# Optimization experiments

Hardware: AMD Instinct MI355X
Metric: run time of the kernel (lower is better)

The kernel has to match this reference:

```python
import jax, jax.numpy as jnp
import numpy as np

B, T, D = 4, 1024, 768
HW = 32            # H = W = sqrt(T)
DS = D // 16       # d_state = 48
CHUNK = 8          # items_each_chunk (must divide W)


def _ln(x, w, b, eps=1e-5):
    mu = x.mean(-1, keepdims=True)
    var = ((x - mu) ** 2).mean(-1, keepdims=True)
    return (x - mu) / jnp.sqrt(var + eps) * w + b


def _conv1x1(x, w):  # x: (B,C,H,W), w: (O,C)
    return jnp.einsum('bchw,oc->bohw', x, w)


def _dwconv(x, w, b, pad):  # depthwise conv, w: (C,1,k,k)
    y = jax.lax.conv_general_dilated(
        x, w, (1, 1), [(pad, pad), (pad, pad)],
        dimension_numbers=('NCHW', 'OIHW', 'NCHW'),
        feature_group_count=x.shape[1])
    if b is not None:
        y = y + b[None, :, None, None]
    return y


def _norm_gates(Gl, Gm, Gr):
    gl, gm, gr = jax.nn.sigmoid(Gl), jax.nn.sigmoid(Gm), jax.nn.sigmoid(Gr)
    s = gl + gm + gr
    s = s.at[:, :, 0, :].set(gm[:, :, 0, :] + gr[:, :, 0, :])    # top row: no h-1 neighbor
    s = s.at[:, :, -1, :].set(gl[:, :, -1, :] + gm[:, :, -1, :])  # bottom row: no h+1 neighbor
    s = jnp.maximum(s, 1e-7)
    return gl / s, gm / s, gr / s


def _gspn_scan(X, L, Gl, Gm, Gr, chunk):
    # GateRecurrent2dnoind: scan along W in independent chunks of `chunk` columns.
    # H[:, :, h, t] = L*X + Gl*Hprev[h-1] + Gm*Hprev[h] + Gr*Hprev[h+1], Hprev=0 at chunk start.
    b, c, h, w = X.shape
    nc = w // chunk

    def to_scan(a):  # (B,C,H,W) -> (chunk, B, C, H, nc)
        return a.reshape(b, c, h, nc, chunk).transpose(4, 0, 1, 2, 3)

    xs, ls, gls, gms, grs = map(to_scan, (X, L, Gl, Gm, Gr))

    def step(hprev, inp):
        x, l, gl, gm, gr = inp
        h_up = jnp.pad(hprev[:, :, :-1], ((0, 0), (0, 0), (1, 0), (0, 0)))
        h_dn = jnp.pad(hprev[:, :, 1:], ((0, 0), (0, 0), (0, 1), (0, 0)))
        hn = l * x + gl * h_up + gm * hprev + gr * h_dn
        return hn, hn

    _, ys = jax.lax.scan(step, jnp.zeros((b, c, h, nc), X.dtype), (xs, ls, gls, gms, grs))
    return ys.transpose(1, 2, 3, 4, 0).reshape(b, c, h, w)


def setup_inputs() -> dict:
    key = jax.random.key(0)
    ks = jax.random.split(key, 16)
    s = 0.02
    return {
        'hidden_states': jax.random.normal(ks[0], (B, T, D), jnp.float32),
        'norm_w': jnp.ones((D,), jnp.float32),
        'norm_b': jnp.zeros((D,), jnp.float32),
        'in_proj_w': jax.random.normal(ks[1], (D, D), jnp.float32) * s,
        'conv7_w': jax.random.normal(ks[2], (D, 1, 7, 7), jnp.float32) * s,
        'conv7_b': jnp.zeros((D,), jnp.float32),
        'xdown_w': jax.random.normal(ks[3], (DS, D), jnp.float32) * s,
        'wup_w': jax.random.normal(ks[4], (12 * D, DS), jnp.float32) * s,
        'lup_w': jax.random.normal(ks[5], (4 * D, DS), jnp.float32) * s,
        'uup_w': jax.random.normal(ks[6], (4 * D, DS), jnp.float32) * s,
        'dcoef_w': jax.random.normal(ks[7], (4 * D, DS), jnp.float32) * s,
        'm_w': jax.random.normal(ks[8], (4,), jnp.float32) * 0.25,
        'outconv_w': jax.random.normal(ks[9], (D, D), jnp.float32) * s,
        'outdconv_w': jax.random.normal(ks[10], (D, 1, 3, 3), jnp.float32) * s,
        'outproj_w': jax.random.normal(ks[11], (D, D), jnp.float32) * s,
    }


def reference(hidden_states, norm_w, norm_b, in_proj_w, conv7_w, conv7_b,
              xdown_w, wup_w, lup_w, uup_w, dcoef_w, m_w,
              outconv_w, outdconv_w, outproj_w):
    b, t, d = hidden_states.shape
    hh = ww = HW
    shortcut = hidden_states
    x = _ln(shortcut, norm_w, norm_b)                      # (B,T,D)
    x = x.transpose(0, 2, 1).reshape(b, d, hh, ww)         # (B,D,H,W)
    x = _conv1x1(x, in_proj_w)
    x = _dwconv(x, conv7_w, conv7_b, 3)
    xp = _conv1x1(x, xdown_w)                              # (B,ds,H,W)
    ws = _conv1x1(xp, wup_w)                               # (B,12D,H,W)
    Ls = _conv1x1(xp, lup_w)                               # (B,4D,H,W)
    Us = _conv1x1(xp, uup_w)
    Ds = _conv1x1(xp, dcoef_w)
    # 4 scan directions: [x, x^T, flip_w(x), flip_w(x^T)]
    x_hwwh = jnp.stack([x, x.transpose(0, 1, 3, 2)], axis=1)       # (B,2,D,H,W)
    xs = jnp.concatenate([x_hwwh, x_hwwh[..., ::-1]], axis=1)      # (B,4,D,H,W)
    xs = xs.reshape(b, 4 * d, hh, ww)
    Gl, Gm, Gr = ws[:, :4 * d], ws[:, 4 * d:8 * d], ws[:, 8 * d:]
    gl, gm, gr = _norm_gates(Gl, Gm, Gr)
    out = _gspn_scan(xs, Ls, gl, gm, gr, CHUNK)
    out = out * Us + xs * Ds
    out = out.reshape(b, 4, d, hh, ww)
    out = jnp.einsum('bkdhw,k->bdhw', out, m_w)            # m_conv (1x1 over 4 dirs)
    out = _conv1x1(out, outconv_w)
    out = _dwconv(out, outdconv_w, None, 1)
    out = out * jax.nn.relu(out)
    out = out.reshape(b, d, t).transpose(0, 2, 1)
    out = out @ outproj_w.T
    return out, shortcut
```

## Files before the change

### kernel.cpp

```cpp
#include <hip/hip_runtime.h>

typedef unsigned short u16;
typedef unsigned int u32;
typedef __attribute__((ext_vector_type(8))) short short8v;
typedef __attribute__((ext_vector_type(4))) float f32x4;

#define DD 768
#define PP 1024
#define NTOK 4096
#define ASN 520

__device__ __forceinline__ u16 f2bf(float f) {
  u32 u = __builtin_bit_cast(u32, f);
  u += 0x7fffu + ((u >> 16) & 1u);
  return (u16)(u >> 16);
}
__device__ __forceinline__ float b2f(u16 v) {
  return __builtin_bit_cast(float, (u32)v << 16);
}
__device__ __forceinline__ float ex8(const short8v& v, int j) {
  const u32 dw = ((const u32*)&v)[j >> 1];
  return __builtin_bit_cast(float, (j & 1) ? (dw & 0xffff0000u) : (dw << 16));
}

__global__ __launch_bounds__(256) void prep_k(const float* __restrict__ win, u16* __restrict__ wInB,
                                              const float* __restrict__ wout, u16* __restrict__ wOutB,
                                              const float* __restrict__ wprj, u16* __restrict__ wPrjB,
                                              const float* __restrict__ xdw, u16* __restrict__ wXdB,
                                              const float* __restrict__ wup, const float* __restrict__ lup,
                                              const float* __restrict__ uup, const float* __restrict__ dco,
                                              u16* __restrict__ wB) {
  const int id = blockIdx.x;
  const int t = threadIdx.x;
  if (id < 6912) {
    const int m = id / 2304;
    const int i = (id - m * 2304) * 256 + t;
    const float* s = (m == 0) ? win : (m == 1) ? wout : wprj;
    u16* d = (m == 0) ? wInB : (m == 1) ? wOutB : wPrjB;
    d[i] = f2bf(s[i]);
  } else if (id < 7104) {
    const int i = (id - 6912) * 256 + t;
    const int r = i / DD;
    wXdB[i] = (r < 48) ? f2bf(xdw[i]) : (u16)0;
  } else {
    const int c = id - 7104;
    u16* dst = wB + (size_t)c * 2048;
    for (int i = t; i < 2048; i += 256) {
      const int row = i >> 6, s = i & 63;
      u16 v = 0;
      if (row < 24 && s < 48) {
        const int k = row & 3, type = row >> 2;
        const int ch = k * DD + c;
        const float* src;
        if (type < 3) src = wup + ((size_t)(type * 3072 + ch)) * 48;
        else if (type == 3) src = lup + (size_t)ch * 48;
        else if (type == 4) src = uup + (size_t)ch * 48;
        else src = dco + (size_t)ch * 48;
        v = f2bf(src[s]);
      }
      dst[i] = v;
    }
  }
}

__global__ __launch_bounds__(256) void ln_k(const float* __restrict__ x,
                                            const float* __restrict__ gw, const float* __restrict__ gb,
                                            u16* __restrict__ lnout, float* __restrict__ shortcut) {
  const int tok = blockIdx.x;
  const int t = threadIdx.x;
  const float* xr = x + (size_t)tok * DD;
  float v0 = xr[t], v1 = xr[t + 256], v2 = xr[t + 512];
  float s = v0 + v1 + v2;
  float q = v0 * v0 + v1 * v1 + v2 * v2;
#pragma unroll
  for (int off = 32; off > 0; off >>= 1) {
    s += __shfl_down(s, off, 64);
    q += __shfl_down(q, off, 64);
  }
  __shared__ float ss[4], qs[4];
  const int wid = t >> 6, lane = t & 63;
  if (lane == 0) { ss[wid] = s; qs[wid] = q; }
  __syncthreads();
  const float st = ss[0] + ss[1] + ss[2] + ss[3];
  const float qt = qs[0] + qs[1] + qs[2] + qs[3];
  const float mu = st * (1.f / 768.f);
  const float var = qt * (1.f / 768.f) - mu * mu;
  const float rstd = rsqrtf(var + 1e-5f);
  float* sc = shortcut + (size_t)tok * DD;
  u16* lo = lnout + (size_t)tok * DD;
  sc[t] = v0; sc[t + 256] = v1; sc[t + 512] = v2;
  lo[t]       = f2bf((v0 - mu) * rstd * gw[t] + gb[t]);
  lo[t + 256] = f2bf((v1 - mu) * rstd * gw[t + 256] + gb[t + 256]);
  lo[t + 512] = f2bf((v2 - mu) * rstd * gw[t + 512] + gb[t + 512]);
}

__global__ __launch_bounds__(256) void gemm_bf16(const u16* __restrict__ A,
                                                 const u16* __restrict__ Bt,
                                                 void* __restrict__ outv, const int mode) {
  __shared__ u16 Al[64][40];
  __shared__ u16 Bl[128][40];
  const int t = threadIdx.x;
  const int ntile = blockIdx.x * 128;
  const int mtile = blockIdx.y * 64;
  const int wid = t >> 6, lane = t & 63;
  const int m0 = (wid & 1) * 32, n0 = (wid >> 1) * 64;
  const int l15 = lane & 15, quad = lane >> 4;
  f32x4 acc[2][4];
#pragma unroll
  for (int mi = 0; mi < 2; ++mi)
#pragma unroll
    for (int ni = 0; ni < 4; ++ni) acc[mi][ni] = (f32x4){0.f, 0.f, 0.f, 0.f};
  const int ra = t >> 2, sa = t & 3;
  const int rb = t >> 1, hb = t & 1;
  const u16* ag = A + (size_t)(mtile + ra) * DD + sa * 8;
  const u16* bg = Bt + (size_t)(ntile + rb) * DD + hb * 16;
  for (int k0 = 0; k0 < DD; k0 += 32) {
    const uint4 av = *reinterpret_cast<const uint4*>(ag + k0);
    const uint4 bv0 = *reinterpret_cast<const uint4*>(bg + k0);
    const uint4 bv1 = *reinterpret_cast<const uint4*>(bg + k0 + 8);
    __syncthreads();
    *reinterpret_cast<uint4*>(&Al[ra][sa * 8]) = av;
    *reinterpret_cast<uint4*>(&Bl[rb][hb * 16]) = bv0;
    *reinterpret_cast<uint4*>(&Bl[rb][hb * 16 + 8]) = bv1;
    __syncthreads();
    short8v af[2];
#pragma unroll
    for (int mi = 0; mi < 2; ++mi)
      af[mi] = *reinterpret_cast<const short8v*>(&Al[m0 + mi * 16 + l15][quad * 8]);
    short8v bfr[4];
#pragma unroll
    for (int ni = 0; ni < 4; ++ni)
      bfr[ni] = *reinterpret_cast<const short8v*>(&Bl[n0 + ni * 16 + l15][quad * 8]);
#pragma unroll
    for (int mi = 0; mi < 2; ++mi)
#pragma unroll
      for (int ni = 0; ni < 4; ++ni)
        acc[mi][ni] = __builtin_amdgcn_mfma_f32_16x16x32_bf16(af[mi], bfr[ni], acc[mi][ni], 0, 0, 0);
  }
#pragma unroll
  for (int mi = 0; mi < 2; ++mi) {
#pragma unroll
    for (int ni = 0; ni < 4; ++ni) {
      const int ob = mtile + m0 + mi * 16 + quad * 4;
      const int pg = ntile + n0 + ni * 16 + l15;
      if (mode == 1) {
        *reinterpret_cast<f32x4*>((float*)outv + (size_t)pg * DD + ob) = acc[mi][ni];
      } else if (mode == 2) {
        const int bb = pg >> 10, pq = pg & 1023;
        const int q = ((pq & 31) >> 4) * 512 + (pq >> 5) * 16 + (pq & 15);
        u16* dst = (u16*)outv + ((size_t)(bb * 1024 + q)) * 64 + ob;
        const u32 lo = (u32)f2bf(acc[mi][ni][0]) | ((u32)f2bf(acc[mi][ni][1]) << 16);
        const u32 hi = (u32)f2bf(acc[mi][ni][2]) | ((u32)f2bf(acc[mi][ni][3]) << 16);
        *reinterpret_cast<uint2*>(dst) = make_uint2(lo, hi);
      } else {
        const int bb = pg >> 10, pq = pg & 1023;
        u16* dstb = (u16*)outv;
#pragma unroll
        for (int r = 0; r < 4; ++r)
          dstb[((size_t)(bb * DD + ob + r)) * PP + pq] = f2bf(acc[mi][ni][r]);
      }
    }
  }
}

__global__ __launch_bounds__(256) void dwconv7_k(const u16* __restrict__ x,
                                                 const float* __restrict__ wgt,
                                                 const float* __restrict__ bias,
                                                 u16* __restrict__ y) {
  const int bc = blockIdx.x;
  const int c = bc % DD;
  __shared__ float tile[38 * 38];
  __shared__ float wl[49];
  __shared__ float bsh[1];
  const int t = threadIdx.x;
  for (int i = t; i < 38 * 38; i += 256) tile[i] = 0.f;
  __syncthreads();
  const u16* xr = x + (size_t)bc * PP;
  for (int i = t; i < 512; i += 256) {
    const u32 v = reinterpret_cast<const u32*>(xr)[i];
    const int p0 = i * 2;
    const int h = p0 >> 5, w = p0 & 31;
    tile[(h + 3) * 38 + w + 3] = b2f((u16)v);
    tile[(h + 3) * 38 + w + 4] = b2f((u16)(v >> 16));
  }
  if (t < 49) wl[t] = wgt[c * 49 + t];
  if (t == 0) bsh[0] = bias[c];
  __syncthreads();
  u16* yo = y + (size_t)bc * PP;
  for (int i = t; i < 1024; i += 256) {
    const int h = i >> 5, w = i & 31;
    float acc = bsh[0];
#pragma unroll
    for (int kh = 0; kh < 7; ++kh)
#pragma unroll
      for (int kw = 0; kw < 7; ++kw)
        acc = fmaf(wl[kh * 7 + kw], tile[(h + kh) * 38 + (w + kw)], acc);
    yo[i] = f2bf(acc);
  }
}

__global__ __launch_bounds__(256) void dwconv3_k(const u16* __restrict__ x,
                                                 const float* __restrict__ wgt,
                                                 u16* __restrict__ y) {
  const int bc = blockIdx.x;
  const int c = bc % DD;
  __shared__ float tile[34 * 34];
  __shared__ float wl[9];
  const int t = threadIdx.x;
  for (int i = t; i < 34 * 34; i += 256) tile[i] = 0.f;
  __syncthreads();
  const u16* xr = x + (size_t)bc * PP;
  for (int i = t; i < 512; i += 256) {
    const u32 v = reinterpret_cast<const u32*>(xr)[i];
    const int p0 = i * 2;
    const int h = p0 >> 5, w = p0 & 31;
    tile[(h + 1) * 34 + w + 1] = b2f((u16)v);
    tile[(h + 1) * 34 + w + 2] = b2f((u16)(v >> 16));
  }
  if (t < 9) wl[t] = wgt[c * 9 + t];
  __syncthreads();
  u16* yo = y + (size_t)bc * PP;
  for (int i = t; i < 1024; i += 256) {
    const int h = i >> 5, w = i & 31;
    float acc = 0.f;
#pragma unroll
    for (int kh = 0; kh < 3; ++kh)
#pragma unroll
      for (int kw = 0; kw < 3; ++kw)
        acc = fmaf(wl[kh * 3 + kw], tile[(h + kh) * 34 + (w + kw)], acc);
    const float r = acc > 0.f ? acc * acc : 0.f;
    yo[i] = f2bf(r);
  }
}

__global__ __launch_bounds__(256, 4) void scan_k(const u16* __restrict__ y2b,
                                                 const u16* __restrict__ xpA,
                                                 const u16* __restrict__ wB,
                                                 const float* __restrict__ mwp,
                                                 u16* __restrict__ out1) {
  const int bid = blockIdx.x;
  const int bc = bid >> 1;
  const int half = bid & 1;
  const int b = bc / DD;
  const int c = bc - b * DD;
  __shared__ u16 act[24 * ASN];
  __shared__ float plane[32][33];
  __shared__ float planeT[32][33];
  __shared__ float outp[2][16][33];
  const int t = threadIdx.x;
  const int wid = t >> 6, lane = t & 63, l15 = lane & 15, quad = lane >> 4;
  {
    const u16* yp = y2b + (size_t)bc * PP;
    for (int i = t; i < 512; i += 256) {
      const u32 v = reinterpret_cast<const u32*>(yp)[i];
      const int p0 = i * 2;
      const int hh = p0 >> 5, ww = p0 & 31;
      const float f0 = b2f((u16)v), f1 = b2f((u16)(v >> 16));
      plane[hh][ww] = f0; plane[hh][ww + 1] = f1;
      planeT[ww][hh] = f0; planeT[ww + 1][hh] = f1;
    }
  }
  {
    const u16* wc = wB + (size_t)c * 2048;
    short8v bw[2][2];
#pragma unroll
    for (int nt = 0; nt < 2; ++nt)
#pragma unroll
      for (int ks = 0; ks < 2; ++ks)
        bw[nt][ks] = *reinterpret_cast<const short8v*>(wc + (nt * 16 + l15) * 64 + ks * 32 + quad * 8);
    const u16* ab = xpA + ((size_t)(b * 1024 + half * 512 + wid * 128)) * 64;
#pragma unroll 4
    for (int mt = 0; mt < 8; ++mt) {
      const u16* ar = ab + (mt * 16 + l15) * 64 + quad * 8;
      const short8v a0 = *reinterpret_cast<const short8v*>(ar);
      const short8v a1 = *reinterpret_cast<const short8v*>(ar + 32);
      f32x4 acc0 = {0.f, 0.f, 0.f, 0.f}, acc1 = {0.f, 0.f, 0.f, 0.f};
      acc0 = __builtin_amdgcn_mfma_f32_16x16x32_bf16(a0, bw[0][0], acc0, 0, 0, 0);
      acc0 = __builtin_amdgcn_mfma_f32_16x16x32_bf16(a1, bw[0][1], acc0, 0, 0, 0);
      acc1 = __builtin_amdgcn_mfma_f32_16x16x32_bf16(a0, bw[1][0], acc1, 0, 0, 0);
      acc1 = __builtin_amdgcn_mfma_f32_16x16x32_bf16(a1, bw[1][1], acc1, 0, 0, 0);
      const int qb = wid * 128 + mt * 16 + quad * 4;
      const u32 lo0 = (u32)f2bf(acc0[0]) | ((u32)f2bf(acc0[1]) << 16);
      const u32 hi0 = (u32)f2bf(acc0[2]) | ((u32)f2bf(acc0[3]) << 16);
      *reinterpret_cast<uint2*>(&act[l15 * ASN + qb]) = make_uint2(lo0, hi0);
      if (l15 < 8) {
        const u32 lo1 = (u32)f2bf(acc1[0]) | ((u32)f2bf(acc1[1]) << 16);
        const u32 hi1 = (u32)f2bf(acc1[2]) | ((u32)f2bf(acc1[3]) << 16);
        *reinterpret_cast<uint2*>(&act[(16 + l15) * ASN + qb]) = make_uint2(lo1, hi1);
      }
    }
  }
  __syncthreads();
  const int dpair = wid & 1;
  const int ncl = wid >> 1;
  const int d = lane >> 5;
  const int h = lane & 31;
  const int k = dpair * 2 + d;
  const float mw = mwp[k];
  const int base16 = h * 16 + ncl * 8;
  const short8v vGl = *reinterpret_cast<const short8v*>(&act[(0  + k) * ASN + base16]);
  const short8v vGm = *reinterpret_cast<const short8v*>(&act[(4  + k) * ASN + base16]);
  const short8v vGr = *reinterpret_cast<const short8v*>(&act[(8  + k) * ASN + base16]);
  const short8v vL  = *reinterpret_cast<const short8v*>(&act[(12 + k) * ASN + base16]);
  const short8v vU  = *reinterpret_cast<const short8v*>(&act[(16 + k) * ASN + base16]);
  const short8v vD  = *reinterpret_cast<const short8v*>(&act[(20 + k) * ASN + base16]);
  const float* prow = (d == 0) ? &plane[h][0] : &planeT[h][0];
  const bool top = (h == 0), bot = (h == 31);
  float H = 0.f;
#pragma unroll
  for (int j = 0; j < 8; ++j) {
    const int w = half * 16 + ncl * 8 + j;
    const int wc_ = dpair ? (31 - w) : w;
    const float xv = prow[wc_];
    float el = __expf(-ex8(vGl, j));
    const float em = __expf(-ex8(vGm, j));
    float er = __expf(-ex8(vGr, j));
    if (top) el = 1e30f;
    if (bot) er = 1e30f;
    const float pl = 1.f + el, pm = 1.f + em, pr = 1.f + er;
    const float ul = pm * pr, um = pl * pr, ur = pl * pm;
    const float rcpS = __builtin_amdgcn_rcpf(ul + um + ur);
    const float up = __shfl(H, lane - 1, 64);
    const float dn = __shfl(H, lane + 1, 64);
    H = fmaf(ex8(vL, j), xv, (fmaf(ul, up, fmaf(um, H, ur * dn))) * rcpS);
    float part = mw * fmaf(H, ex8(vU, j), xv * ex8(vD, j));
    part += __shfl_xor(part, 32, 64);
    if (d == 0) outp[dpair][ncl * 8 + j][h] = part;
  }
  __syncthreads();
  const int hh = t >> 3, wp = t & 7;
  const float v0 = outp[0][wp * 2][hh] + outp[1][wp * 2][hh];
  const float v1 = outp[0][wp * 2 + 1][hh] + outp[1][wp * 2 + 1][hh];
  const u32 pk = (u32)f2bf(v0) | ((u32)f2bf(v1) << 16);
  *reinterpret_cast<u32*>(out1 + (size_t)bc * PP + hh * 32 + half * 16 + wp * 2) = pk;
}

__global__ __launch_bounds__(256) void transpose_bf16(const u16* __restrict__ in,
                                                      u16* __restrict__ out) {
  __shared__ u16 tile[64][72];
  const int b = blockIdx.z;
  const int c0 = blockIdx.y * 64;
  const int p0 = blockIdx.x * 64;
  const int t = threadIdx.x;
  const int r = t >> 2, s2 = t & 3;
  const u16* src = in + ((size_t)(b * DD + c0 + r)) * PP + p0 + s2 * 16;
  *reinterpret_cast<uint4*>(&tile[r][s2 * 16]) = *reinterpret_cast<const uint4*>(src);
  *reinterpret_cast<uint4*>(&tile[r][s2 * 16 + 8]) = *reinterpret_cast<const uint4*>(src + 8);
  __syncthreads();
  const int pr = t >> 2, cs = t & 3;
  union { u16 u[16]; uint4 v[2]; } vals;
#pragma unroll
  for (int i = 0; i < 16; ++i) vals.u[i] = tile[cs * 16 + i][pr];
  u16* dst = out + ((size_t)(b * 1024 + p0 + pr)) * DD + c0 + cs * 16;
  reinterpret_cast<uint4*>(dst)[0] = vals.v[0];
  reinterpret_cast<uint4*>(dst)[1] = vals.v[1];
}

extern "C" void kernel_launch(void* const* d_in, const int* in_sizes, int n_in,
                              void* d_out, int out_size, void* d_ws, size_t ws_size,
                              hipStream_t stream) {
  const float* hs   = (const float*)d_in[0];
  const float* nw   = (const float*)d_in[1];
  const float* nb   = (const float*)d_in[2];
  const float* win  = (const float*)d_in[3];
  const float* c7w  = (const float*)d_in[4];
  const float* c7b  = (const float*)d_in[5];
  const float* xdw  = (const float*)d_in[6];
  const float* wupw = (const float*)d_in[7];
  const float* lupw = (const float*)d_in[8];
  const float* uupw = (const float*)d_in[9];
  const float* dcow = (const float*)d_in[10];
  const float* mww  = (const float*)d_in[11];
  const float* wout = (const float*)d_in[12];
  const float* odw  = (const float*)d_in[13];
  const float* wprj = (const float*)d_in[14];
  float* out0 = (float*)d_out;
  float* shortcut = out0 + (size_t)NTOK * DD;

  char* ws = (char*)d_ws;
  u16* lnA    = (u16*)(ws + 0);
  u16* wInB   = (u16*)(ws + 6291456);
  u16* wOutB  = (u16*)(ws + 7471104);
  u16* wPrjB  = (u16*)(ws + 8650752);
  u16* wB     = (u16*)(ws + 9830400);
  u16* wXdB   = (u16*)(ws + 12976128);
  u16* xpA    = (u16*)(ws + 13074432);
  u16* y1b    = (u16*)(ws + 13598720);
  u16* y2b    = (u16*)(ws + 19890176);
  u16* y2t    = (u16*)(ws + 26181632);
  u16* out1   = (u16*)(ws + 32473088);
  u16* out1T  = lnA;
  u16* y3b    = y1b;
  u16* y4b    = y2b;
  u16* y4T    = y2t;

  prep_k<<<7872, 256, 0, stream>>>(win, wInB, wout, wOutB, wprj, wPrjB,
                                   xdw, wXdB, wupw, lupw, uupw, dcow, wB);
  ln_k<<<4096, 256, 0, stream>>>(hs, nw, nb, lnA, shortcut);
  gemm_bf16<<<dim3(32, 12), 256, 0, stream>>>(wInB, lnA, y1b, 3);
  dwconv7_k<<<3072, 256, 0, stream>>>(y1b, c7w, c7b, y2b);
  transpose_bf16<<<dim3(16, 12, 4), 256, 0, stream>>>(y2b, y2t);
  gemm_bf16<<<dim3(32, 1), 256, 0, stream>>>(wXdB, y2t, xpA, 2);
  scan_k<<<6144, 256, 0, stream>>>(y2b, xpA, wB, mww, out1);
  transpose_bf16<<<dim3(16, 12, 4), 256, 0, stream>>>(out1, out1T);
  gemm_bf16<<<dim3(32, 12), 256, 0, stream>>>(wOutB, out1T, y3b, 3);
  dwconv3_k<<<3072, 256, 0, stream>>>(y3b, odw, y4b);
  transpose_bf16<<<dim3(16, 12, 4), 256, 0, stream>>>(y4b, y4T);
  gemm_bf16<<<dim3(32, 12), 256, 0, stream>>>(wPrjB, y4T, out0, 1);
}
```

Measured before the change: 268.0 us.

## Merge LN into weight prep and slim scan kernel shared memory and inner loop

Folds the layernorm kernel into the weight-conversion prep kernel so one launch is saved. In the scan kernel, the input planes and output partials move from fp32 to bf16 in shared memory, and the launch bound is raised so more blocks can fit per CU. Gate normalization and L*x are precomputed ahead of the serial shuffle recurrence, which shortens the dependent chain per step. Round-to-nearest bf16 conversion is replaced by truncation via a byte permute, and the output partials are stored as truncated bf16, which adds rounding error.

```diff
diff --git a/kernel.cpp b/kernel.cpp
--- a/kernel.cpp
+++ b/kernel.cpp
@@ -18,32 +18,67 @@
 __device__ __forceinline__ float b2f(u16 v) {
   return __builtin_bit_cast(float, (u32)v << 16);
 }
+__device__ __forceinline__ u32 pk_trunc(float fa, float fb) {
+  return __builtin_amdgcn_perm(__builtin_bit_cast(u32, fa), __builtin_bit_cast(u32, fb), 0x07060302u);
+}
 __device__ __forceinline__ float ex8(const short8v& v, int j) {
   const u32 dw = ((const u32*)&v)[j >> 1];
   return __builtin_bit_cast(float, (j & 1) ? (dw & 0xffff0000u) : (dw << 16));
 }
 
-__global__ __launch_bounds__(256) void prep_k(const float* __restrict__ win, u16* __restrict__ wInB,
-                                              const float* __restrict__ wout, u16* __restrict__ wOutB,
-                                              const float* __restrict__ wprj, u16* __restrict__ wPrjB,
-                                              const float* __restrict__ xdw, u16* __restrict__ wXdB,
-                                              const float* __restrict__ wup, const float* __restrict__ lup,
-                                              const float* __restrict__ uup, const float* __restrict__ dco,
-                                              u16* __restrict__ wB) {
+__global__ __launch_bounds__(256) void prep_ln_k(const float* __restrict__ hs,
+                                                 const float* __restrict__ gw, const float* __restrict__ gb,
+                                                 u16* __restrict__ lnout, float* __restrict__ shortcut,
+                                                 const float* __restrict__ win, u16* __restrict__ wInB,
+                                                 const float* __restrict__ wout, u16* __restrict__ wOutB,
+                                                 const float* __restrict__ wprj, u16* __restrict__ wPrjB,
+                                                 const float* __restrict__ xdw, u16* __restrict__ wXdB,
+                                                 const float* __restrict__ wup, const float* __restrict__ lup,
+                                                 const float* __restrict__ uup, const float* __restrict__ dco,
+                                                 u16* __restrict__ wB) {
   const int id = blockIdx.x;
   const int t = threadIdx.x;
-  if (id < 6912) {
-    const int m = id / 2304;
-    const int i = (id - m * 2304) * 256 + t;
+  if (id < 4096) {
+    const int tok = id;
+    const float* xr = hs + (size_t)tok * DD;
+    float v0 = xr[t], v1 = xr[t + 256], v2 = xr[t + 512];
+    float s = v0 + v1 + v2;
+    float q = v0 * v0 + v1 * v1 + v2 * v2;
+#pragma unroll
+    for (int off = 32; off > 0; off >>= 1) {
+      s += __shfl_down(s, off, 64);
+      q += __shfl_down(q, off, 64);
+    }
+    __shared__ float ss[4], qs[4];
+    const int wid = t >> 6, lane = t & 63;
+    if (lane == 0) { ss[wid] = s; qs[wid] = q; }
+    __syncthreads();
+    const float st = ss[0] + ss[1] + ss[2] + ss[3];
+    const float qt = qs[0] + qs[1] + qs[2] + qs[3];
+    const float mu = st * (1.f / 768.f);
+    const float var = qt * (1.f / 768.f) - mu * mu;
+    const float rstd = rsqrtf(var + 1e-5f);
+    float* sc = shortcut + (size_t)tok * DD;
+    u16* lo = lnout + (size_t)tok * DD;
+    sc[t] = v0; sc[t + 256] = v1; sc[t + 512] = v2;
+    lo[t]       = f2bf((v0 - mu) * rstd * gw[t] + gb[t]);
+    lo[t + 256] = f2bf((v1 - mu) * rstd * gw[t + 256] + gb[t + 256]);
+    lo[t + 512] = f2bf((v2 - mu) * rstd * gw[t + 512] + gb[t + 512]);
+    return;
+  }
+  const int id2 = id - 4096;
+  if (id2 < 6912) {
+    const int m = id2 / 2304;
+    const int i = (id2 - m * 2304) * 256 + t;
     const float* s = (m == 0) ? win : (m == 1) ? wout : wprj;
     u16* d = (m == 0) ? wInB : (m == 1) ? wOutB : wPrjB;
     d[i] = f2bf(s[i]);
-  } else if (id < 7104) {
-    const int i = (id - 6912) * 256 + t;
+  } else if (id2 < 7104) {
+    const int i = (id2 - 6912) * 256 + t;
     const int r = i / DD;
     wXdB[i] = (r < 48) ? f2bf(xdw[i]) : (u16)0;
   } else {
-    const int c = id - 7104;
+    const int c = id2 - 7104;
     u16* dst = wB + (size_t)c * 2048;
     for (int i = t; i < 2048; i += 256) {
       const int row = i >> 6, s = i & 63;
@@ -63,37 +98,6 @@
   }
 }
 
-__global__ __launch_bounds__(256) void ln_k(const float* __restrict__ x,
-                                            const float* __restrict__ gw, const float* __restrict__ gb,
-                                            u16* __restrict__ lnout, float* __restrict__ shortcut) {
-  const int tok = blockIdx.x;
-  const int t = threadIdx.x;
-  const float* xr = x + (size_t)tok * DD;
-  float v0 = xr[t], v1 = xr[t + 256], v2 = xr[t + 512];
-  float s = v0 + v1 + v2;
-  float q = v0 * v0 + v1 * v1 + v2 * v2;
-#pragma unroll
-  for (int off = 32; off > 0; off >>= 1) {
-    s += __shfl_down(s, off, 64);
-    q += __shfl_down(q, off, 64);
-  }
-  __shared__ float ss[4], qs[4];
-  const int wid = t >> 6, lane = t & 63;
-  if (lane == 0) { ss[wid] = s; qs[wid] = q; }
-  __syncthreads();
-  const float st = ss[0] + ss[1] + ss[2] + ss[3];
-  const float qt = qs[0] + qs[1] + qs[2] + qs[3];
-  const float mu = st * (1.f / 768.f);
-  const float var = qt * (1.f / 768.f) - mu * mu;
-  const float rstd = rsqrtf(var + 1e-5f);
-  float* sc = shortcut + (size_t)tok * DD;
-  u16* lo = lnout + (size_t)tok * DD;
-  sc[t] = v0; sc[t + 256] = v1; sc[t + 512] = v2;
-  lo[t]       = f2bf((v0 - mu) * rstd * gw[t] + gb[t]);
-  lo[t + 256] = f2bf((v1 - mu) * rstd * gw[t + 256] + gb[t + 256]);
-  lo[t + 512] = f2bf((v2 - mu) * rstd * gw[t + 512] + gb[t + 512]);
-}
-
 __global__ __launch_bounds__(256) void gemm_bf16(const u16* __restrict__ A,
                                                  const u16* __restrict__ Bt,
                                                  void* __restrict__ outv, const int mode) {
@@ -233,7 +237,7 @@
   }
 }
 
-__global__ __launch_bounds__(256, 4) void scan_k(const u16* __restrict__ y2b,
+__global__ __launch_bounds__(256, 5) void scan_k(const u16* __restrict__ y2b,
                                                  const u16* __restrict__ xpA,
                                                  const u16* __restrict__ wB,
                                                  const float* __restrict__ mwp,
@@ -244,9 +248,9 @@
   const int b = bc / DD;
   const int c = bc - b * DD;
   __shared__ u16 act[24 * ASN];
-  __shared__ float plane[32][33];
-  __shared__ float planeT[32][33];
-  __shared__ float outp[2][16][33];
+  __shared__ u16 planeb[32][34];
+  __shared__ u16 planeTb[32][34];
+  __shared__ u16 outpb[2][16][34];
   const int t = threadIdx.x;
   const int wid = t >> 6, lane = t & 63, l15 = lane & 15, quad = lane >> 4;
   {
@@ -255,9 +259,9 @@
       const u32 v = reinterpret_cast<const u32*>(yp)[i];
       const int p0 = i * 2;
       const int hh = p0 >> 5, ww = p0 & 31;
-      const float f0 = b2f((u16)v), f1 = b2f((u16)(v >> 16));
-      plane[hh][ww] = f0; plane[hh][ww + 1] = f1;
-      planeT[ww][hh] = f0; planeT[ww + 1][hh] = f1;
+      *reinterpret_cast<u32*>(&planeb[hh][ww]) = v;
+      planeTb[ww][hh] = (u16)v;
+      planeTb[ww + 1][hh] = (u16)(v >> 16);
     }
   }
   {
@@ -280,14 +284,11 @@
       acc1 = __builtin_amdgcn_mfma_f32_16x16x32_bf16(a0, bw[1][0], acc1, 0, 0, 0);
       acc1 = __builtin_amdgcn_mfma_f32_16x16x32_bf16(a1, bw[1][1], acc1, 0, 0, 0);
       const int qb = wid * 128 + mt * 16 + quad * 4;
-      const u32 lo0 = (u32)f2bf(acc0[0]) | ((u32)f2bf(acc0[1]) << 16);
-      const u32 hi0 = (u32)f2bf(acc0[2]) | ((u32)f2bf(acc0[3]) << 16);
-      *reinterpret_cast<uint2*>(&act[l15 * ASN + qb]) = make_uint2(lo0, hi0);
-      if (l15 < 8) {
-        const u32 lo1 = (u32)f2bf(acc1[0]) | ((u32)f2bf(acc1[1]) << 16);
-        const u32 hi1 = (u32)f2bf(acc1[2]) | ((u32)f2bf(acc1[3]) << 16);
-        *reinterpret_cast<uint2*>(&act[(16 + l15) * ASN + qb]) = make_uint2(lo1, hi1);
-      }
+      *reinterpret_cast<uint2*>(&act[l15 * ASN + qb]) =
+          make_uint2(pk_trunc(acc0[1], acc0[0]), pk_trunc(acc0[3], acc0[2]));
+      if (l15 < 8)
+        *reinterpret_cast<uint2*>(&act[(16 + l15) * ASN + qb]) =
+            make_uint2(pk_trunc(acc1[1], acc1[0]), pk_trunc(acc1[3], acc1[2]));
     }
   }
   __syncthreads();
@@ -304,14 +305,14 @@
   const short8v vL  = *reinterpret_cast<const short8v*>(&act[(12 + k) * ASN + base16]);
   const short8v vU  = *reinterpret_cast<const short8v*>(&act[(16 + k) * ASN + base16]);
   const short8v vD  = *reinterpret_cast<const short8v*>(&act[(20 + k) * ASN + base16]);
-  const float* prow = (d == 0) ? &plane[h][0] : &planeT[h][0];
+  const u16* prow = (d == 0) ? &planeb[h][0] : &planeTb[h][0];
   const bool top = (h == 0), bot = (h == 31);
-  float H = 0.f;
+  float gl[8], gm[8], gr[8], Lx[8], xvv[8];
 #pragma unroll
   for (int j = 0; j < 8; ++j) {
     const int w = half * 16 + ncl * 8 + j;
     const int wc_ = dpair ? (31 - w) : w;
-    const float xv = prow[wc_];
+    const float xv = b2f(prow[wc_]);
     float el = __expf(-ex8(vGl, j));
     const float em = __expf(-ex8(vGm, j));
     float er = __expf(-ex8(vGr, j));
@@ -320,18 +321,26 @@
     const float pl = 1.f + el, pm = 1.f + em, pr = 1.f + er;
     const float ul = pm * pr, um = pl * pr, ur = pl * pm;
     const float rcpS = __builtin_amdgcn_rcpf(ul + um + ur);
+    gl[j] = ul * rcpS; gm[j] = um * rcpS; gr[j] = ur * rcpS;
+    Lx[j] = ex8(vL, j) * xv;
+    xvv[j] = xv;
+  }
+  float H = 0.f;
+#pragma unroll
+  for (int j = 0; j < 8; ++j) {
     const float up = __shfl(H, lane - 1, 64);
     const float dn = __shfl(H, lane + 1, 64);
-    H = fmaf(ex8(vL, j), xv, (fmaf(ul, up, fmaf(um, H, ur * dn))) * rcpS);
-    float part = mw * fmaf(H, ex8(vU, j), xv * ex8(vD, j));
+    H = fmaf(gl[j], up, fmaf(gm[j], H, fmaf(gr[j], dn, Lx[j])));
+    float part = fmaf(H, ex8(vU, j), xvv[j] * ex8(vD, j)) * mw;
     part += __shfl_xor(part, 32, 64);
-    if (d == 0) outp[dpair][ncl * 8 + j][h] = part;
+    if (d == 0)
+      outpb[dpair][ncl * 8 + j][h] = (u16)(__builtin_bit_cast(u32, part) >> 16);
   }
   __syncthreads();
   const int hh = t >> 3, wp = t & 7;
-  const float v0 = outp[0][wp * 2][hh] + outp[1][wp * 2][hh];
-  const float v1 = outp[0][wp * 2 + 1][hh] + outp[1][wp * 2 + 1][hh];
-  const u32 pk = (u32)f2bf(v0) | ((u32)f2bf(v1) << 16);
+  const float v0 = b2f(outpb[0][wp * 2][hh]) + b2f(outpb[1][wp * 2][hh]);
+  const float v1 = b2f(outpb[0][wp * 2 + 1][hh]) + b2f(outpb[1][wp * 2 + 1][hh]);
+  const u32 pk = pk_trunc(v1, v0);
   *reinterpret_cast<u32*>(out1 + (size_t)bc * PP + hh * 32 + half * 16 + wp * 2) = pk;
 }
 
@@ -394,9 +403,9 @@
   u16* y4b    = y2b;
   u16* y4T    = y2t;
 
-  prep_k<<<7872, 256, 0, stream>>>(win, wInB, wout, wOutB, wprj, wPrjB,
-                                   xdw, wXdB, wupw, lupw, uupw, dcow, wB);
-  ln_k<<<4096, 256, 0, stream>>>(hs, nw, nb, lnA, shortcut);
+  prep_ln_k<<<11968, 256, 0, stream>>>(hs, nw, nb, lnA, shortcut,
+                                       win, wInB, wout, wOutB, wprj, wPrjB,
+                                       xdw, wXdB, wupw, lupw, uupw, dcow, wB);
   gemm_bf16<<<dim3(32, 12), 256, 0, stream>>>(wInB, lnA, y1b, 3);
   dwconv7_k<<<3072, 256, 0, stream>>>(y1b, c7w, c7b, y2b);
   transpose_bf16<<<dim3(16, 12, 4), 256, 0, stream>>>(y2b, y2t);
```

Result: no change. 263.0 us (-1.9%).
